# Kernel optimization log

Measured on AMD Instinct MI355X. Metric: run time of the kernel, lower is better.

Reference implementation:

```python
import jax, jax.numpy as jnp
import numpy as np

SCORE_THR = 0.5
RADII = jnp.array([0.5, 0.6, 0.7], dtype=jnp.float32)  # radius_dict[c]; all labels 0..C-1 covered

B, N, C = 2, 8192, 3


def setup_inputs() -> dict:
    key = jax.random.key(0)
    k1, k2 = jax.random.split(key)
    xyz = jax.random.normal(k1, (B, N, 3), dtype=jnp.float32)
    cls_features = jax.random.normal(k2, (B, N, C), dtype=jnp.float32)
    return {"xyz": xyz, "cls_features": cls_features}


def _greedy_select(xyz, cls_features):
    """Greedy per-class radius suppression over the flattened batch.
    Returns sample_idx (B, L) int32, zero-padded exactly like the torch code
    (sample_idx is zeros except slot i of the batch owning selection i)."""
    b, n, _ = xyz.shape
    L = b * n
    scores = jax.nn.sigmoid(jnp.max(cls_features, axis=2))   # (B, N)
    labels = jnp.argmax(cls_features, axis=2)                # (B, N)
    valid = scores >= SCORE_THR

    flat_scores = jnp.where(valid, scores, -jnp.inf).reshape(L)
    order = jnp.argsort(-flat_scores)                        # descending score; invalid sink to end
    sorted_labels = labels.reshape(L)[order]
    sorted_valid = valid.reshape(L)[order]
    sorted_batch = (order // n).astype(jnp.int32)
    sorted_pts = xyz.reshape(L, 3)[order]

    def cond(state):
        i, remaining, _ = state
        return remaining.any() & (i < L)

    def body(state):
        i, remaining, sel_pos = state
        cur = jnp.argmax(remaining)                  # first remaining point in sorted order
        # NB: faithful to the original bug: radius chosen via sorted_labels[i]
        # (loop counter), not the label of the current point.
        r = RADII[sorted_labels[i]]
        d2 = jnp.sum((sorted_pts - sorted_pts[cur]) ** 2, axis=-1)  # (L,)
        suppress = (sorted_batch == sorted_batch[cur]) & (d2 <= r * r)
        return (i + 1, remaining & ~suppress, sel_pos.at[i].set(cur.astype(jnp.int32)))

    sel0 = jnp.full((L,), -1, dtype=jnp.int32)
    _, _, sel_pos = jax.lax.while_loop(cond, body, (jnp.int32(0), sorted_valid, sel0))

    picked = sel_pos >= 0
    orig = jnp.where(picked, order[jnp.maximum(sel_pos, 0)], 0)  # flat index in [0, L)
    bidx = jnp.where(picked, orig // n, 0)
    pidx = jnp.where(picked, orig % n, 0)
    slots = jnp.arange(L)
    # zeros init + scatter exactly mirrors torch: sample_idx[batch, i] = point
    sample_idx = jnp.zeros((b, L), dtype=jnp.int32).at[bidx, slots].set(pidx.astype(jnp.int32))
    return sample_idx


def reference(xyz, cls_features):
    sample_idx = _greedy_select(xyz, cls_features)
    bsz = xyz.shape[0]
    # gather_operation: new_xyz[b, m] = xyz[b, sample_idx[b, m]]
    new_xyz = xyz[jnp.arange(bsz)[:, None], sample_idx]          # (B, L, 3)
    return new_xyz, sample_idx
```

## Files before the change

kernel.cpp:

```cpp
#include <hip/hip_runtime.h>
#include <stdint.h>


#define L_TOT 16384
#define NPT   8192

__device__ __forceinline__ int cellco(float v) {
    int c = (int)floorf((v + 6.4f) * 1.25f);
    return c < 0 ? 0 : (c > 15 ? 15 : c);
}
__device__ __forceinline__ float d2f(float ax, float ay, float az,
                                     float bx, float by, float bz) {
    float dx = __fsub_rn(ax, bx), dy = __fsub_rn(ay, by), dz = __fsub_rn(az, bz);
    return __fadd_rn(__fadd_rn(__fmul_rn(dx, dx), __fmul_rn(dy, dy)), __fmul_rn(dz, dz));
}

__global__ void k1_keys(const float* __restrict__ cls, uint64_t* __restrict__ keys,
                        uint8_t* __restrict__ umeta, uint16_t* __restrict__ sample,
                        int* __restrict__ cellcnt) {
    int l = blockIdx.x * blockDim.x + threadIdx.x;
    if (l >= L_TOT) return;
    ((uint32_t*)sample)[l] = 0;
    if (l < 8192) cellcnt[l] = 0;
    float c0 = cls[l * 3 + 0], c1 = cls[l * 3 + 1], c2 = cls[l * 3 + 2];
    float m = c0; int lab = 0;
    if (c1 > m) { m = c1; lab = 1; }
    if (c2 > m) { m = c2; lab = 2; }
    int valid = (m >= 0.0f) ? 1 : 0;
    float keyf = valid ? m : -__builtin_inff();
    uint32_t u = __float_as_uint(keyf);
    uint32_t o = (u & 0x80000000u) ? ~u : (u | 0x80000000u);
    keys[l] = ((uint64_t)(~o) << 32) | (uint32_t)l;
    umeta[l] = (uint8_t)(lab | (valid << 2));
}

__global__ void __launch_bounds__(256) k2_sort(
    const uint64_t* __restrict__ keys, const uint8_t* __restrict__ umeta,
    const float* __restrict__ xyz,
    float4* __restrict__ spts, uint8_t* __restrict__ slab, uint16_t* __restrict__ sorder,
    int* __restrict__ cellcnt) {
    __shared__ uint64_t tile[2048];
    __shared__ int psum[256];
    const int t = threadIdx.x;
    const int elem = t & 31, part = t >> 5;
    const int l = blockIdx.x * 32 + elem;
    const uint64_t myk = keys[l];
    int cnt = 0;
    for (int t0 = 0; t0 < L_TOT; t0 += 2048) {
        for (int j = t; j < 2048; j += 256) tile[j] = keys[t0 + j];
        __syncthreads();
        const int b0 = part * 256;
        #pragma unroll 4
        for (int j = 0; j < 256; ++j) cnt += (tile[b0 + j] < myk) ? 1 : 0;
        __syncthreads();
    }
    psum[t] = cnt;
    __syncthreads();
    if (t < 32) {
        int rank = 0;
        #pragma unroll
        for (int q = 0; q < 8; ++q) rank += psum[q * 32 + t];
        const int ll = blockIdx.x * 32 + t;
        int b = ll >> 13, p = ll & (NPT - 1);
        const float* src = xyz + ((size_t)(b * NPT + p)) * 3;
        float x = src[0], y = src[1], z = src[2];
        uint8_t mt = umeta[ll];
        int lab = mt & 3, valid = (mt >> 2) & 1;
        float4 v; v.x = x; v.y = y; v.z = z;
        v.w = __uint_as_float((uint32_t)(b | (valid << 1)));
        spts[rank] = v;
        slab[rank] = (uint8_t)lab;
        sorder[rank] = (uint16_t)ll;
        if (valid) {
            int cl = (b << 12) | (cellco(z) << 8) | (cellco(y) << 4) | cellco(x);
            atomicAdd(&cellcnt[cl], 1);
        }
    }
}

__global__ void g2_scan(int* __restrict__ cellcnt, int* __restrict__ cellstart) {
    __shared__ int part[256];
    __shared__ int poff[256];
    int t = threadIdx.x;
    int base = t * 32;
    int loc[32];
    int s = 0;
    for (int k = 0; k < 32; ++k) { loc[k] = cellcnt[base + k]; s += loc[k]; }
    part[t] = s;
    __syncthreads();
    if (t == 0) {
        int run = 0;
        for (int q = 0; q < 256; ++q) { poff[q] = run; run += part[q]; }
    }
    __syncthreads();
    int run = poff[t];
    for (int k = 0; k < 32; ++k) {
        cellstart[base + k] = run; run += loc[k];
        cellcnt[base + k] = 0;
    }
    if (t == 255) cellstart[8192] = run;
}

__global__ void g3_scatter(const float4* __restrict__ spts, const int* __restrict__ cellstart,
                           int* __restrict__ cellfill, float4* __restrict__ cellxyz) {
    int pos = blockIdx.x * blockDim.x + threadIdx.x;
    if (pos >= L_TOT) return;
    float4 v = spts[pos];
    uint32_t w = __float_as_uint(v.w);
    if (!(w & 2u)) return;
    int b = (int)(w & 1u);
    int cl = (b << 12) | (cellco(v.z) << 8) | (cellco(v.y) << 4) | cellco(v.x);
    int slot = atomicAdd(&cellfill[cl], 1);
    float4 o; o.x = v.x; o.y = v.y; o.z = v.z; o.w = __uint_as_float((uint32_t)pos);
    cellxyz[cellstart[cl] + slot] = o;
}

__global__ void __launch_bounds__(1024) k3_greedy(
    const float4* __restrict__ spts, const uint8_t* __restrict__ slab,
    const uint16_t* __restrict__ sorder,
    const int* __restrict__ cellstart, const float4* __restrict__ cellxyz,
    uint16_t* __restrict__ sample) {
    __shared__ uint32_t rem[512];
    __shared__ uint16_t cs16[8193];
    __shared__ float4   pkd[4][128];
    __shared__ int      pkb[4][128];
    __shared__ int      pkn[4];
    __shared__ int      win_pos[128];
    __shared__ int      s_done;

    const int t = threadIdx.x;
    const int V = cellstart[8192];
    for (int j = t; j < 8193; j += 1024) cs16[j] = (uint16_t)cellstart[j];
    for (int w = t; w < 512; w += 1024) {
        int lo = w * 32;
        uint32_t m;
        if (V >= lo + 32) m = 0xFFFFFFFFu;
        else if (V <= lo) m = 0u;
        else m = (1u << (V - lo)) - 1u;
        rem[w] = m;
    }
    if (t < 4) pkn[t] = 0;
    if (t == 0) s_done = 0;
    __syncthreads();

    float4 cv0 = make_float4(0,0,0,0), cv1 = make_float4(0,0,0,0);
    int cord0 = 0, cord1 = 0, cb0 = 0, cb1 = 0;
    float cr0 = 0.f, cr1 = 0.f;
    int ii = 0, nwin = 0;

    auto gather = [&]() {
        uint32_t wv[8]; int cnt = 0;
        #pragma unroll
        for (int q = 0; q < 8; ++q) {
            wv[q] = ((volatile uint32_t*)rem)[t * 8 + q];
            cnt += __popc(wv[q]);
        }
        int pre = cnt;
        #pragma unroll
        for (int off = 1; off < 64; off <<= 1) {
            int nb = __shfl_up(pre, off);
            if (t >= off) pre += nb;
        }
        const int total = __shfl(pre, 63);
        if (total == 0) { if (t == 0) s_done = 1; nwin = 0; return; }
        int r = pre - cnt;
        uint32_t clr[8];
        #pragma unroll
        for (int q = 0; q < 8; ++q) clr[q] = 0u;
        if (r < 128) {
            #pragma unroll
            for (int q = 0; q < 8; ++q) {
                if (r >= 128) break;
                uint32_t m = wv[q];
                while (m && r < 128) {
                    uint32_t bit = m & (~m + 1u);
                    int b = __builtin_ctz(m);
                    m &= m - 1u;
                    win_pos[r] = (t * 8 + q) * 32 + b;
                    clr[q] |= bit;
                    ++r;
                }
            }
        }
        #pragma unroll
        for (int q = 0; q < 8; ++q)
            if (clr[q]) atomicAnd(&rem[t * 8 + q], ~clr[q]);
        for (int z = total + t; z < 128; z += 64) win_pos[z] = 0;
        __builtin_amdgcn_wave_barrier();
        asm volatile("s_waitcnt lgkmcnt(0)" ::: "memory");
        __builtin_amdgcn_wave_barrier();
        nwin = total < 128 ? total : 128;
        int p0 = win_pos[t], p1 = win_pos[64 + t];
        cv0 = spts[p0]; cv1 = spts[p1];
        cord0 = (int)sorder[p0]; cord1 = (int)sorder[p1];
        cb0 = cord0 >> 13; cb1 = cord1 >> 13;
        int o0 = ii + t;       o0 = o0 > (L_TOT - 1) ? (L_TOT - 1) : o0;
        int o1 = ii + 64 + t;  o1 = o1 > (L_TOT - 1) ? (L_TOT - 1) : o1;
        int l0 = slab[o0], l1 = slab[o1];
        float rr0 = (l0 == 0) ? 0.5f : ((l0 == 1) ? 0.6f : 0.7f);
        float rr1 = (l1 == 0) ? 0.5f : ((l1 == 1) ? 0.6f : 0.7f);
        cr0 = __fmul_rn(rr0, rr0); cr1 = __fmul_rn(rr1, rr1);
    };

    if (t < 64) gather();
    __syncthreads();

    for (int ph = 0; ph < 4096; ++ph) {
        const int cur = ph & 3, prev1 = (ph + 3) & 3, prev2 = (ph + 2) & 3;
        if (t < 64) {
            int np = 0;
            if (nwin > 0) {
                bool a0 = (t < nwin), a1 = (64 + t < nwin);
                #pragma unroll 1
                for (int rs = 0; rs < 2; ++rs) {
                    const int ring = (rs == 0) ? prev1 : prev2;
                    const int m = pkn[ring];
                    for (int j = 0; j < m; ++j) {
                        float4 pk = pkd[ring][j];
                        int pb = pkb[ring][j];
                        if (a0 && cb0 == pb &&
                            d2f(cv0.x, cv0.y, cv0.z, pk.x, pk.y, pk.z) <= pk.w) a0 = false;
                        if (a1 && cb1 == pb &&
                            d2f(cv1.x, cv1.y, cv1.z, pk.x, pk.y, pk.z) <= pk.w) a1 = false;
                    }
                }
                unsigned long long am0 = __ballot(a0 ? 1 : 0);
                unsigned long long am1 = __ballot(a1 ? 1 : 0);
                while (am0 | am1) {
                    const int js = am0 ? 0 : 1;
                    const int jl = am0 ? (int)__builtin_ctzll(am0)
                                       : (int)__builtin_ctzll(am1);
                    float px = __shfl(js ? cv1.x : cv0.x, jl);
                    float py = __shfl(js ? cv1.y : cv0.y, jl);
                    float pz = __shfl(js ? cv1.z : cv0.z, jl);
                    int   pb = __shfl(js ? cb1 : cb0, jl);
                    float r2 = __shfl((np & 64) ? cr1 : cr0, np & 63);
                    if (t == jl) {
                        int    b_ = js ? cb1 : cb0;
                        int    o_ = js ? cord1 : cord0;
                        float  x_ = js ? cv1.x : cv0.x;
                        float  y_ = js ? cv1.y : cv0.y;
                        float  z_ = js ? cv1.z : cv0.z;
                        pkd[cur][np] = make_float4(x_, y_, z_, r2);
                        pkb[cur][np] = b_;
                        sample[b_ * L_TOT + ii + np] = (uint16_t)(o_ & (NPT - 1));
                    }
                    if (a0 && cb0 == pb && d2f(cv0.x, cv0.y, cv0.z, px, py, pz) <= r2) a0 = false;
                    if (a1 && cb1 == pb && d2f(cv1.x, cv1.y, cv1.z, px, py, pz) <= r2) a1 = false;
                    ++np;
                    am0 = __ballot(a0 ? 1 : 0);
                    am1 = __ballot(a1 ? 1 : 0);
                }
                ii += np;
            }
            if (t == 0) pkn[cur] = np;
            gather();
        } else {
            const int np = pkn[prev1];
            if (np > 0) {
                const int tid = t - 64;
                const int ntask = np * 216;
                for (int task = tid; task < ntask; task += 960) {
                    int sub = task & 7;
                    int pc = task >> 3;
                    int p = pc / 27;
                    int c = pc - p * 27;
                    float4 pv = pkd[prev1][p];
                    int pb_ = pkb[prev1][p];
                    float r2 = pv.w;
                    int cx = cellco(pv.x) + (c % 3) - 1;
                    int cy = cellco(pv.y) + ((c / 3) % 3) - 1;
                    int cz = cellco(pv.z) + (c / 9) - 1;
                    if ((unsigned)cx > 15u || (unsigned)cy > 15u || (unsigned)cz > 15u) continue;
                    float lox = -6.4f + 0.8f * cx, hix = lox + 0.8f;
                    float loy = -6.4f + 0.8f * cy, hiy = loy + 0.8f;
                    float loz = -6.4f + 0.8f * cz, hiz = loz + 0.8f;
                    if (cx == 0) lox = -1e30f;  if (cx == 15) hix = 1e30f;
                    if (cy == 0) loy = -1e30f;  if (cy == 15) hiy = 1e30f;
                    if (cz == 0) loz = -1e30f;  if (cz == 15) hiz = 1e30f;
                    float dx = fmaxf(fmaxf(lox - pv.x, pv.x - hix), 0.0f);
                    float dy = fmaxf(fmaxf(loy - pv.y, pv.y - hiy), 0.0f);
                    float dz = fmaxf(fmaxf(loz - pv.z, pv.z - hiz), 0.0f);
                    if (dx * dx + dy * dy + dz * dz > r2 + 0.02f) continue;
                    int st = (int)cs16[(pb_ << 12) | (cz << 8) | (cy << 4) | cx];
                    int en = (int)cs16[((pb_ << 12) | (cz << 8) | (cy << 4) | cx) + 1];
                    for (int k = st + sub; k < en; k += 8) {
                        float4 q = cellxyz[k];
                        float d2 = d2f(q.x, q.y, q.z, pv.x, pv.y, pv.z);
                        if (d2 <= r2) {
                            uint32_t qp = __float_as_uint(q.w);
                            atomicAnd(&rem[qp >> 5], ~(1u << (qp & 31)));
                        }
                    }
                }
            }
        }
        __syncthreads();
        if (s_done) break;
    }
}

__global__ void k4_out(const float* __restrict__ xyz, const uint16_t* __restrict__ sample,
                       float* __restrict__ out) {
    int s = blockIdx.x * blockDim.x + threadIdx.x;
    if (s >= 2 * L_TOT) return;
    int idx = (int)sample[s];
    int b = s >> 14;
    const float* src = xyz + ((size_t)(b * NPT + idx)) * 3;
    float* dst = out + (size_t)s * 3;
    dst[0] = src[0]; dst[1] = src[1]; dst[2] = src[2];
    out[3 * 2 * L_TOT + s] = (float)idx;
}

extern "C" void kernel_launch(void* const* d_in, const int* in_sizes, int n_in,
                              void* d_out, int out_size, void* d_ws, size_t ws_size,
                              hipStream_t stream) {
    const float* xyz = (const float*)d_in[0];
    const float* cls = (const float*)d_in[1];
    float* out = (float*)d_out;
    char* ws = (char*)d_ws;
    float4*   spts    = (float4*)  (ws + 0);
    uint8_t*  slab    = (uint8_t*) (ws + 262144);
    uint16_t* sorder  = (uint16_t*)(ws + 278528);
    int*      cellcnt = (int*)     (ws + 311296);
    int*      cellst  = (int*)     (ws + 344064);
    float4*   cellxyz = (float4*)  (ws + 380928);
    uint64_t* keys    = (uint64_t*)(ws + 380928);
    uint8_t*  umeta   = (uint8_t*) (ws + 512000);
    uint16_t* sample  = (uint16_t*)(ws + 643072);

    k1_keys   <<<64,  256, 0, stream>>>(cls, keys, umeta, sample, cellcnt);
    k2_sort   <<<512, 256, 0, stream>>>(keys, umeta, xyz, spts, slab, sorder, cellcnt);
    g2_scan   <<<1,   256, 0, stream>>>(cellcnt, cellst);
    g3_scatter<<<64,  256, 0, stream>>>(spts, cellst, cellcnt, cellxyz);
    k3_greedy <<<1,  1024, 0, stream>>>(spts, slab, sorder, cellst, cellxyz, sample);
    k4_out    <<<128, 256, 0, stream>>>(xyz, sample, out);
}
```

Baseline: 630.8 us.

## Replace dynamic window gather with fixed sorted-order windows and double buffering

The greedy kernel no longer compacts the remaining-point bitmask into a 128-entry window each phase with a prefix scan. It now walks fixed consecutive 128-point blocks of the sorted order and reads the remaining bits directly, prefetching the next block's points during the current phase. Checking only the previous phase's picks is enough because earlier picks' suppression has already been applied to rem, so the pick ring shrinks from 4 to 2. Labels are staged in LDS and the early-exit flag is removed, so the loop always runs ceil(V/128) phases even when most points are already suppressed.

```diff
diff --git a/kernel.cpp b/kernel.cpp
--- a/kernel.cpp
+++ b/kernel.cpp
@@ -13,6 +13,10 @@
                                      float bx, float by, float bz) {
     float dx = __fsub_rn(ax, bx), dy = __fsub_rn(ay, by), dz = __fsub_rn(az, bz);
     return __fadd_rn(__fadd_rn(__fmul_rn(dx, dx), __fmul_rn(dy, dy)), __fmul_rn(dz, dz));
+}
+__device__ __forceinline__ float rad2(int lb) {
+    float rr = (lb == 0) ? 0.5f : ((lb == 1) ? 0.6f : 0.7f);
+    return __fmul_rn(rr, rr);
 }
 
 __global__ void k1_keys(const float* __restrict__ cls, uint64_t* __restrict__ keys,
@@ -122,15 +126,23 @@
     uint16_t* __restrict__ sample) {
     __shared__ uint32_t rem[512];
     __shared__ uint16_t cs16[8193];
-    __shared__ float4   pkd[4][128];
-    __shared__ int      pkb[4][128];
-    __shared__ int      pkn[4];
-    __shared__ int      win_pos[128];
-    __shared__ int      s_done;
+    __shared__ uint8_t  slds[L_TOT];
+    __shared__ float4   pkd[2][128];
+    __shared__ int      pkb[2][128];
+    __shared__ int      pkn[2];
 
     const int t = threadIdx.x;
     const int V = cellstart[8192];
+    const int NPH = (V + 127) >> 7;
+
+    float4 cv0 = make_float4(0,0,0,0), cv1 = make_float4(0,0,0,0);
+    int cord0 = 0, cord1 = 0;
+    if (t < 64) {
+        cv0 = spts[t]; cv1 = spts[64 + t];
+        cord0 = (int)sorder[t]; cord1 = (int)sorder[64 + t];
+    }
     for (int j = t; j < 8193; j += 1024) cs16[j] = (uint16_t)cellstart[j];
+    for (int j = t; j < L_TOT; j += 1024) slds[j] = slab[j];
     for (int w = t; w < 512; w += 1024) {
         int lo = w * 32;
         uint32_t m;
@@ -139,124 +151,70 @@
         else m = (1u << (V - lo)) - 1u;
         rem[w] = m;
     }
-    if (t < 4) pkn[t] = 0;
-    if (t == 0) s_done = 0;
-    __syncthreads();
-
-    float4 cv0 = make_float4(0,0,0,0), cv1 = make_float4(0,0,0,0);
-    int cord0 = 0, cord1 = 0, cb0 = 0, cb1 = 0;
-    float cr0 = 0.f, cr1 = 0.f;
-    int ii = 0, nwin = 0;
-
-    auto gather = [&]() {
-        uint32_t wv[8]; int cnt = 0;
-        #pragma unroll
-        for (int q = 0; q < 8; ++q) {
-            wv[q] = ((volatile uint32_t*)rem)[t * 8 + q];
-            cnt += __popc(wv[q]);
-        }
-        int pre = cnt;
-        #pragma unroll
-        for (int off = 1; off < 64; off <<= 1) {
-            int nb = __shfl_up(pre, off);
-            if (t >= off) pre += nb;
-        }
-        const int total = __shfl(pre, 63);
-        if (total == 0) { if (t == 0) s_done = 1; nwin = 0; return; }
-        int r = pre - cnt;
-        uint32_t clr[8];
-        #pragma unroll
-        for (int q = 0; q < 8; ++q) clr[q] = 0u;
-        if (r < 128) {
-            #pragma unroll
-            for (int q = 0; q < 8; ++q) {
-                if (r >= 128) break;
-                uint32_t m = wv[q];
-                while (m && r < 128) {
-                    uint32_t bit = m & (~m + 1u);
-                    int b = __builtin_ctz(m);
-                    m &= m - 1u;
-                    win_pos[r] = (t * 8 + q) * 32 + b;
-                    clr[q] |= bit;
-                    ++r;
+    if (t < 2) pkn[t] = 0;
+    __syncthreads();
+
+    int ii = 0;
+    for (int ph = 0; ph < NPH; ++ph) {
+        const int cur = ph & 1, prv = cur ^ 1;
+        if (t < 64) {
+            const int nb = (ph + 1) << 7;
+            int q0 = nb + t;       q0 = q0 > (L_TOT - 1) ? (L_TOT - 1) : q0;
+            int q1 = nb + 64 + t;  q1 = q1 > (L_TOT - 1) ? (L_TOT - 1) : q1;
+            float4 nv0 = spts[q0], nv1 = spts[q1];
+            int nord0 = (int)sorder[q0], nord1 = (int)sorder[q1];
+
+            int o0 = ii + t;      o0 = o0 > (L_TOT - 1) ? (L_TOT - 1) : o0;
+            int o1 = ii + 64 + t; o1 = o1 > (L_TOT - 1) ? (L_TOT - 1) : o1;
+            float cr0 = rad2((int)slds[o0]);
+            float cr1 = rad2((int)slds[o1]);
+
+            const int pos0 = (ph << 7) + t, pos1 = pos0 + 64;
+            bool a0 = (pos0 < V) && ((rem[pos0 >> 5] >> (pos0 & 31)) & 1u);
+            bool a1 = (pos1 < V) && ((rem[pos1 >> 5] >> (pos1 & 31)) & 1u);
+            const int cb0 = cord0 >> 13, cb1 = cord1 >> 13;
+            const int m = pkn[prv];
+            for (int j = 0; j < m; ++j) {
+                float4 pk = pkd[prv][j];
+                int pb = pkb[prv][j];
+                if (a0 && cb0 == pb &&
+                    d2f(cv0.x, cv0.y, cv0.z, pk.x, pk.y, pk.z) <= pk.w) a0 = false;
+                if (a1 && cb1 == pb &&
+                    d2f(cv1.x, cv1.y, cv1.z, pk.x, pk.y, pk.z) <= pk.w) a1 = false;
+            }
+            unsigned long long am0 = __ballot(a0 ? 1 : 0);
+            unsigned long long am1 = __ballot(a1 ? 1 : 0);
+            int np = 0;
+            const int ii0 = ii;
+            while (am0 | am1) {
+                const int js = am0 ? 0 : 1;
+                const int jl = (int)__builtin_ctzll(am0 ? am0 : am1);
+                float px = __shfl(js ? cv1.x : cv0.x, jl);
+                float py = __shfl(js ? cv1.y : cv0.y, jl);
+                float pz = __shfl(js ? cv1.z : cv0.z, jl);
+                int   pb = __shfl(js ? cb1 : cb0, jl);
+                float r2 = (np & 64) ? __shfl(cr1, np & 63) : __shfl(cr0, np & 63);
+                if (t == jl) {
+                    float x_ = js ? cv1.x : cv0.x;
+                    float y_ = js ? cv1.y : cv0.y;
+                    float z_ = js ? cv1.z : cv0.z;
+                    int   b_ = js ? cb1 : cb0;
+                    int   o_ = js ? cord1 : cord0;
+                    pkd[cur][np] = make_float4(x_, y_, z_, r2);
+                    pkb[cur][np] = b_;
+                    sample[b_ * L_TOT + ii0 + np] = (uint16_t)(o_ & (NPT - 1));
                 }
+                if (a0 && cb0 == pb && d2f(cv0.x, cv0.y, cv0.z, px, py, pz) <= r2) a0 = false;
+                if (a1 && cb1 == pb && d2f(cv1.x, cv1.y, cv1.z, px, py, pz) <= r2) a1 = false;
+                ++np;
+                am0 = __ballot(a0 ? 1 : 0);
+                am1 = __ballot(a1 ? 1 : 0);
             }
-        }
-        #pragma unroll
-        for (int q = 0; q < 8; ++q)
-            if (clr[q]) atomicAnd(&rem[t * 8 + q], ~clr[q]);
-        for (int z = total + t; z < 128; z += 64) win_pos[z] = 0;
-        __builtin_amdgcn_wave_barrier();
-        asm volatile("s_waitcnt lgkmcnt(0)" ::: "memory");
-        __builtin_amdgcn_wave_barrier();
-        nwin = total < 128 ? total : 128;
-        int p0 = win_pos[t], p1 = win_pos[64 + t];
-        cv0 = spts[p0]; cv1 = spts[p1];
-        cord0 = (int)sorder[p0]; cord1 = (int)sorder[p1];
-        cb0 = cord0 >> 13; cb1 = cord1 >> 13;
-        int o0 = ii + t;       o0 = o0 > (L_TOT - 1) ? (L_TOT - 1) : o0;
-        int o1 = ii + 64 + t;  o1 = o1 > (L_TOT - 1) ? (L_TOT - 1) : o1;
-        int l0 = slab[o0], l1 = slab[o1];
-        float rr0 = (l0 == 0) ? 0.5f : ((l0 == 1) ? 0.6f : 0.7f);
-        float rr1 = (l1 == 0) ? 0.5f : ((l1 == 1) ? 0.6f : 0.7f);
-        cr0 = __fmul_rn(rr0, rr0); cr1 = __fmul_rn(rr1, rr1);
-    };
-
-    if (t < 64) gather();
-    __syncthreads();
-
-    for (int ph = 0; ph < 4096; ++ph) {
-        const int cur = ph & 3, prev1 = (ph + 3) & 3, prev2 = (ph + 2) & 3;
-        if (t < 64) {
-            int np = 0;
-            if (nwin > 0) {
-                bool a0 = (t < nwin), a1 = (64 + t < nwin);
-                #pragma unroll 1
-                for (int rs = 0; rs < 2; ++rs) {
-                    const int ring = (rs == 0) ? prev1 : prev2;
-                    const int m = pkn[ring];
-                    for (int j = 0; j < m; ++j) {
-                        float4 pk = pkd[ring][j];
-                        int pb = pkb[ring][j];
-                        if (a0 && cb0 == pb &&
-                            d2f(cv0.x, cv0.y, cv0.z, pk.x, pk.y, pk.z) <= pk.w) a0 = false;
-                        if (a1 && cb1 == pb &&
-                            d2f(cv1.x, cv1.y, cv1.z, pk.x, pk.y, pk.z) <= pk.w) a1 = false;
-                    }
-                }
-                unsigned long long am0 = __ballot(a0 ? 1 : 0);
-                unsigned long long am1 = __ballot(a1 ? 1 : 0);
-                while (am0 | am1) {
-                    const int js = am0 ? 0 : 1;
-                    const int jl = am0 ? (int)__builtin_ctzll(am0)
-                                       : (int)__builtin_ctzll(am1);
-                    float px = __shfl(js ? cv1.x : cv0.x, jl);
-                    float py = __shfl(js ? cv1.y : cv0.y, jl);
-                    float pz = __shfl(js ? cv1.z : cv0.z, jl);
-                    int   pb = __shfl(js ? cb1 : cb0, jl);
-                    float r2 = __shfl((np & 64) ? cr1 : cr0, np & 63);
-                    if (t == jl) {
-                        int    b_ = js ? cb1 : cb0;
-                        int    o_ = js ? cord1 : cord0;
-                        float  x_ = js ? cv1.x : cv0.x;
-                        float  y_ = js ? cv1.y : cv0.y;
-                        float  z_ = js ? cv1.z : cv0.z;
-                        pkd[cur][np] = make_float4(x_, y_, z_, r2);
-                        pkb[cur][np] = b_;
-                        sample[b_ * L_TOT + ii + np] = (uint16_t)(o_ & (NPT - 1));
-                    }
-                    if (a0 && cb0 == pb && d2f(cv0.x, cv0.y, cv0.z, px, py, pz) <= r2) a0 = false;
-                    if (a1 && cb1 == pb && d2f(cv1.x, cv1.y, cv1.z, px, py, pz) <= r2) a1 = false;
-                    ++np;
-                    am0 = __ballot(a0 ? 1 : 0);
-                    am1 = __ballot(a1 ? 1 : 0);
-                }
-                ii += np;
-            }
+            ii = ii0 + np;
             if (t == 0) pkn[cur] = np;
-            gather();
+            cv0 = nv0; cv1 = nv1; cord0 = nord0; cord1 = nord1;
         } else {
-            const int np = pkn[prev1];
+            const int np = pkn[prv];
             if (np > 0) {
                 const int tid = t - 64;
                 const int ntask = np * 216;
@@ -265,8 +223,8 @@
                     int pc = task >> 3;
                     int p = pc / 27;
                     int c = pc - p * 27;
-                    float4 pv = pkd[prev1][p];
-                    int pb_ = pkb[prev1][p];
+                    float4 pv = pkd[prv][p];
+                    int pb_ = pkb[prv][p];
                     float r2 = pv.w;
                     int cx = cellco(pv.x) + (c % 3) - 1;
                     int cy = cellco(pv.y) + ((c / 3) % 3) - 1;
@@ -282,8 +240,9 @@
                     float dy = fmaxf(fmaxf(loy - pv.y, pv.y - hiy), 0.0f);
                     float dz = fmaxf(fmaxf(loz - pv.z, pv.z - hiz), 0.0f);
                     if (dx * dx + dy * dy + dz * dz > r2 + 0.02f) continue;
-                    int st = (int)cs16[(pb_ << 12) | (cz << 8) | (cy << 4) | cx];
-                    int en = (int)cs16[((pb_ << 12) | (cz << 8) | (cy << 4) | cx) + 1];
+                    int cl = (pb_ << 12) | (cz << 8) | (cy << 4) | cx;
+                    int st = (int)cs16[cl];
+                    int en = (int)cs16[cl + 1];
                     for (int k = st + sub; k < en; k += 8) {
                         float4 q = cellxyz[k];
                         float d2 = d2f(q.x, q.y, q.z, pv.x, pv.y, pv.z);
@@ -296,7 +255,6 @@
             }
         }
         __syncthreads();
-        if (s_done) break;
     }
 }
 
```

Result: slower. 654.5 us (+3.8%).
